# Optimization experiments

Measured on AMD Instinct MI355X. Metric: run time of the kernel, lower is better.

## Reference

```python
import jax, jax.numpy as jnp
import numpy as np

IN_F = 1024
OUT_F = 1024

def setup_inputs() -> dict:
    key = jax.random.key(0)
    ks = jax.random.split(key, 7)
    s = 1.0 / np.sqrt(IN_F)
    x = jax.random.normal(ks[0], (4, 2048, IN_F), dtype=jnp.float32)
    Wq = jax.random.uniform(ks[1], (OUT_F, IN_F), jnp.float32, -s, s)
    bq = jax.random.uniform(ks[2], (OUT_F,), jnp.float32, -s, s)
    Wk = jax.random.uniform(ks[3], (OUT_F, IN_F), jnp.float32, -s, s)
    bk = jax.random.uniform(ks[4], (OUT_F,), jnp.float32, -s, s)
    Wv = jax.random.uniform(ks[5], (OUT_F, IN_F), jnp.float32, -s, s)
    bv = jax.random.uniform(ks[6], (OUT_F,), jnp.float32, -s, s)
    return {"x": x, "Wq": Wq, "bq": bq, "Wk": Wk, "bk": bk, "Wv": Wv, "bv": bv}

def reference(x, Wq, bq, Wk, bk, Wv, bv):
    # Projector: ReLU(Linear(x))
    q = jax.nn.relu(jnp.einsum('bsd,od->bso', x, Wq) + bq)  # [B,S,O]
    k = jax.nn.relu(jnp.einsum('bsd,od->bso', x, Wk) + bk)
    v = jax.nn.relu(jnp.einsum('bsd,od->bso', x, Wv) + bv)
    logits = jnp.einsum('bio,bko->bik', q, k)  # unscaled QK^T, [B,S,S]
    scores = jax.nn.softmax(logits, axis=-1)
    out = jnp.einsum('bik,bko->bio', scores, v)
    return out
```

## Files before the change

kernel.cpp:

```cpp
#include <hip/hip_runtime.h>
#include <hip/hip_bf16.h>


#define SEQ 2048
#define DIM 1024
#define NB 4
#define MTOT (NB * SEQ)

typedef __attribute__((ext_vector_type(8))) short frag_ab;
typedef __attribute__((ext_vector_type(16))) float frag_c16;

__device__ __forceinline__ ushort f2bf(float f) {
    union { float f; unsigned u; } x; x.f = f;
    unsigned r = x.u + 0x7fffu + ((x.u >> 16) & 1u);
    return (ushort)(r >> 16);
}

typedef __attribute__((address_space(1))) const unsigned int guint;
typedef __attribute__((address_space(3))) unsigned int luint;

__device__ __forceinline__ void gld_lds16(const void* g, void* l) {
    __builtin_amdgcn_global_load_lds((guint*)g, (luint*)l, 16, 0, 0);
}

__device__ __forceinline__ void gemm_tiles(
    const ushort* __restrict__ A, size_t lda,
    const ushort* __restrict__ B, size_t ldb, int K,
    ushort* As, ushort* Bs, frag_c16 (&acc)[2][2])
{
    const int tid  = threadIdx.x;
    const int wave = tid >> 6;
    const int lane = tid & 63;
    const int l32  = lane & 31;
    const int half = lane >> 5;
    const int rin  = lane >> 3;
    const int cp   = lane & 7;
    const int cl   = cp ^ rin;
    const int wm = (wave & 1) * 64;
    const int wn = (wave >> 1) * 64;

    for (int k0 = 0; k0 < K; k0 += 64) {
        #pragma unroll
        for (int g = 0; g < 4; ++g) {
            int qc  = g * 4 + wave;
            int row = qc * 8 + rin;
            gld_lds16(A + (size_t)row * lda + k0 + cl * 8, As + qc * 512);
            gld_lds16(B + (size_t)row * ldb + k0 + cl * 8, Bs + qc * 512);
        }
        __syncthreads();
        frag_ab af[2][4], bf[2][4];
        #pragma unroll
        for (int mi = 0; mi < 2; ++mi) {
            int row = wm + mi * 32 + l32;
            int sw = row & 7;
            #pragma unroll
            for (int ks = 0; ks < 4; ++ks) {
                int c = (ks * 2 + half) ^ sw;
                af[mi][ks] = *(const frag_ab*)&As[row * 64 + c * 8];
            }
        }
        #pragma unroll
        for (int ni = 0; ni < 2; ++ni) {
            int row = wn + ni * 32 + l32;
            int sw = row & 7;
            #pragma unroll
            for (int ks = 0; ks < 4; ++ks) {
                int c = (ks * 2 + half) ^ sw;
                bf[ni][ks] = *(const frag_ab*)&Bs[row * 64 + c * 8];
            }
        }
        #pragma unroll
        for (int ks = 0; ks < 4; ++ks)
            #pragma unroll
            for (int mi = 0; mi < 2; ++mi)
                #pragma unroll
                for (int ni = 0; ni < 2; ++ni)
                    acc[mi][ni] = __builtin_amdgcn_mfma_f32_32x32x16_bf16(
                        af[mi][ks], bf[ni][ks], acc[mi][ni], 0, 0, 0);
        __syncthreads();
    }
}


#define NX4 (MTOT * DIM / 4)
#define NW4 (DIM * DIM / 4)
__global__ __launch_bounds__(256) void cvt_kernel(
    const float* __restrict__ x,
    const float* __restrict__ Wq, const float* __restrict__ Wk,
    const float* __restrict__ Wv,
    ushort* __restrict__ xb, ushort* __restrict__ Wb)
{
    size_t i = (size_t)blockIdx.x * 256 + threadIdx.x;
    const float* src; ushort* dst; size_t idx;
    if (i < NX4) { src = x; dst = xb; idx = i; }
    else {
        size_t j = i - NX4;
        int w = (int)(j >> 18);
        idx = j & (NW4 - 1);
        src = w == 0 ? Wq : (w == 1 ? Wk : Wv);
        dst = Wb + (size_t)w * DIM * DIM;
    }
    float4 f = ((const float4*)src)[idx];
    ushort4 u; u.x = f2bf(f.x); u.y = f2bf(f.y); u.z = f2bf(f.z); u.w = f2bf(f.w);
    ((ushort4*)dst)[idx] = u;
}

__global__ __launch_bounds__(256) void qkv_kernel(
    const ushort* __restrict__ xb, const ushort* __restrict__ Wb,
    const float* __restrict__ bq, const float* __restrict__ bk,
    const float* __restrict__ bv,
    ushort* __restrict__ q, ushort* __restrict__ kk, ushort* __restrict__ vt)
{
    const float* bias;
    if (blockIdx.z == 0)      bias = bq;
    else if (blockIdx.z == 1) bias = bk;
    else                      bias = bv;
    const ushort* W = Wb + (size_t)blockIdx.z * DIM * DIM;

    __shared__ ushort As[128 * 64];
    __shared__ ushort Bs[128 * 64];

    const int tid  = threadIdx.x;
    const int wave = tid >> 6;
    const int lane = tid & 63;
    const int l32  = lane & 31;
    const int half = lane >> 5;
    const int m0 = blockIdx.x * 128;
    const int n0 = blockIdx.y * 128;
    const int wm = (wave & 1) * 64;
    const int wn = (wave >> 1) * 64;

    frag_c16 acc[2][2] = {};
    gemm_tiles(xb + (size_t)m0 * DIM, DIM, W + (size_t)n0 * DIM, DIM, DIM,
               As, Bs, acc);

    if (blockIdx.z == 2) {
        const int bz = m0 >> 11;
        const int sb = (m0 & (SEQ - 1)) + wm;
        #pragma unroll
        for (int ni = 0; ni < 2; ++ni) {
            int col = n0 + wn + ni * 32 + l32;
            float bb = bias[col];
            ushort* vrow = vt + ((size_t)(bz * DIM + col)) * SEQ;
            #pragma unroll
            for (int mi = 0; mi < 2; ++mi)
                #pragma unroll
                for (int g = 0; g < 4; ++g) {
                    int s0 = sb + mi * 32 + 8 * g + 4 * half;
                    ushort4 u;
                    #pragma unroll
                    for (int j = 0; j < 4; ++j) {
                        float val = acc[mi][ni][4 * g + j] + bb;
                        val = val > 0.0f ? val : 0.0f;
                        ((ushort*)&u)[j] = f2bf(val);
                    }
                    *(ushort4*)&vrow[s0] = u;
                }
        }
    } else {
        ushort* out = blockIdx.z == 0 ? q : kk;
        #pragma unroll
        for (int ni = 0; ni < 2; ++ni) {
            int col = n0 + wn + ni * 32 + l32;
            float bb = bias[col];
            #pragma unroll
            for (int mi = 0; mi < 2; ++mi)
                #pragma unroll
                for (int r = 0; r < 16; ++r) {
                    int row = m0 + wm + mi * 32 + (r & 3) + 8 * (r >> 2) + 4 * half;
                    float val = acc[mi][ni][r] + bb;
                    val = val > 0.0f ? val : 0.0f;
                    out[(size_t)row * DIM + col] = f2bf(val);
                }
        }
    }
}

__global__ __launch_bounds__(256) void qk_kernel(
    const ushort* __restrict__ q, const ushort* __restrict__ kk,
    float* __restrict__ logits)
{
    __shared__ ushort As[128 * 64];
    __shared__ ushort Bs[128 * 64];

    const int tid  = threadIdx.x;
    const int wave = tid >> 6;
    const int lane = tid & 63;
    const int l32  = lane & 31;
    const int half = lane >> 5;
    const int bz = blockIdx.z;
    const int m0 = blockIdx.x * 128;
    const int n0 = blockIdx.y * 128;
    const int wm = (wave & 1) * 64;
    const int wn = (wave >> 1) * 64;
    const size_t base = (size_t)bz * SEQ;

    frag_c16 acc[2][2] = {};
    gemm_tiles(q + (base + m0) * DIM, DIM, kk + (base + n0) * DIM, DIM, DIM,
               As, Bs, acc);

    #pragma unroll
    for (int mi = 0; mi < 2; ++mi)
        #pragma unroll
        for (int r = 0; r < 16; ++r) {
            int row = m0 + wm + mi * 32 + (r & 3) + 8 * (r >> 2) + 4 * half;
            #pragma unroll
            for (int ni = 0; ni < 2; ++ni) {
                int col = n0 + wn + ni * 32 + l32;
                logits[(base + row) * SEQ + col] = acc[mi][ni][r];
            }
        }
}

__global__ __launch_bounds__(256) void softmax_kernel(float* __restrict__ logits)
{
    const int row  = blockIdx.x * 4 + (threadIdx.x >> 6);
    const int lane = threadIdx.x & 63;
    float* p = logits + (size_t)row * SEQ;

    float4 x[8];
    #pragma unroll
    for (int i = 0; i < 8; ++i) x[i] = ((const float4*)p)[lane + 64 * i];

    float m = -3.4e38f;
    #pragma unroll
    for (int i = 0; i < 8; ++i)
        m = fmaxf(m, fmaxf(fmaxf(x[i].x, x[i].y), fmaxf(x[i].z, x[i].w)));
    #pragma unroll
    for (int off = 32; off; off >>= 1) m = fmaxf(m, __shfl_xor(m, off, 64));

    float s = 0.0f;
    #pragma unroll
    for (int i = 0; i < 8; ++i) {
        x[i].x = __expf(x[i].x - m); x[i].y = __expf(x[i].y - m);
        x[i].z = __expf(x[i].z - m); x[i].w = __expf(x[i].w - m);
        s += (x[i].x + x[i].y) + (x[i].z + x[i].w);
    }
    #pragma unroll
    for (int off = 32; off; off >>= 1) s += __shfl_xor(s, off, 64);
    float inv = 1.0f / s;

    ushort* o = (ushort*)p;
    #pragma unroll
    for (int i = 0; i < 8; ++i) {
        ushort4 u;
        u.x = f2bf(x[i].x * inv); u.y = f2bf(x[i].y * inv);
        u.z = f2bf(x[i].z * inv); u.w = f2bf(x[i].w * inv);
        ((ushort4*)o)[lane + 64 * i] = u;
    }
}

__global__ __launch_bounds__(256) void pv_kernel(
    const ushort* __restrict__ probs, const ushort* __restrict__ vt,
    float* __restrict__ out)
{
    __shared__ ushort As[128 * 64];
    __shared__ ushort Bs[128 * 64];

    const int tid  = threadIdx.x;
    const int wave = tid >> 6;
    const int lane = tid & 63;
    const int l32  = lane & 31;
    const int half = lane >> 5;
    const int bz = blockIdx.z;
    const int m0 = blockIdx.x * 128;
    const int n0 = blockIdx.y * 128;
    const int wm = (wave & 1) * 64;
    const int wn = (wave >> 1) * 64;

    frag_c16 acc[2][2] = {};
    gemm_tiles(probs + ((size_t)(bz * SEQ + m0)) * 4096, 4096,
               vt + ((size_t)(bz * DIM + n0)) * SEQ, SEQ, SEQ,
               As, Bs, acc);

    #pragma unroll
    for (int mi = 0; mi < 2; ++mi)
        #pragma unroll
        for (int r = 0; r < 16; ++r) {
            int row = m0 + wm + mi * 32 + (r & 3) + 8 * (r >> 2) + 4 * half;
            #pragma unroll
            for (int ni = 0; ni < 2; ++ni) {
                int col = n0 + wn + ni * 32 + l32;
                out[((size_t)(bz * SEQ + row)) * DIM + col] = acc[mi][ni][r];
            }
        }
}

extern "C" void kernel_launch(void* const* d_in, const int* in_sizes, int n_in,
                              void* d_out, int out_size, void* d_ws, size_t ws_size,
                              hipStream_t stream)
{
    const float* x  = (const float*)d_in[0];
    const float* Wq = (const float*)d_in[1];
    const float* bq = (const float*)d_in[2];
    const float* Wk = (const float*)d_in[3];
    const float* bk = (const float*)d_in[4];
    const float* Wv = (const float*)d_in[5];
    const float* bv = (const float*)d_in[6];
    float* out = (float*)d_out;

    char* ws = (char*)d_ws;
    ushort* q      = (ushort*)(ws);
    ushort* kk     = (ushort*)(ws + ((size_t)16 << 20));
    ushort* vt     = (ushort*)(ws + ((size_t)48 << 20));
    float*  logits = (float*) (ws + ((size_t)64 << 20));
    ushort* xb     = (ushort*)(ws + ((size_t)64 << 20));
    ushort* Wb     = (ushort*)(ws + ((size_t)80 << 20));

    cvt_kernel<<<dim3((NX4 + 3 * NW4) / 256), 256, 0, stream>>>(
        x, Wq, Wk, Wv, xb, Wb);

    qkv_kernel<<<dim3(MTOT / 128, DIM / 128, 3), 256, 0, stream>>>(
        xb, Wb, bq, bk, bv, q, kk, vt);
    qk_kernel<<<dim3(SEQ / 128, SEQ / 128, NB), 256, 0, stream>>>(q, kk, logits);
    softmax_kernel<<<NB * SEQ / 4, 256, 0, stream>>>(logits);
    pv_kernel<<<dim3(SEQ / 128, DIM / 128, NB), 256, 0, stream>>>(
        (const ushort*)logits, vt, out);
}
```

Before: 265.3 us.

## Use 256x256 tiles with double-buffered async LDS pipeline in GEMM kernels

Replaces the 128x128 single-buffer GEMM core with a 256x256 tile computed by 8 waves, double-buffered LDS, and staged global-to-LDS loads issued ahead of the MFMA phases with explicit vmcnt waits and raw barriers. Wave priority is raised around MFMA bursts. The intent is to overlap memory loads with matrix math and to raise arithmetic intensity per tile. In exchange it uses 128KB of LDS per block, fewer blocks (grid shrinks 4x), and relies on hand-counted vmcnt ordering that could be fragile.

New measurement: 293.4 us. 10.6% more time.

```diff
diff --git a/kernel.cpp b/kernel.cpp
--- a/kernel.cpp
+++ b/kernel.cpp
@@ -23,62 +23,120 @@
     __builtin_amdgcn_global_load_lds((guint*)g, (luint*)l, 16, 0, 0);
 }
 
-__device__ __forceinline__ void gemm_tiles(
+__device__ __forceinline__ void bar() {
+    asm volatile("" ::: "memory");
+    __builtin_amdgcn_s_barrier();
+    asm volatile("" ::: "memory");
+}
+#define VMCNT(n) asm volatile("s_waitcnt vmcnt(" #n ")" ::: "memory")
+
+#define TS (256 * 64)
+
+__device__ __forceinline__ void stage64(const ushort* __restrict__ P,
+                                        size_t ld, int k0, ushort* dst,
+                                        int row0, int wave, int lane)
+{
+    int row = row0 + wave * 8 + (lane >> 3);
+    int cl  = (lane & 7) ^ (row & 7);
+    gld_lds16(P + (size_t)row * ld + k0 + cl * 8, dst + (row0 + wave * 8) * 64);
+}
+
+__device__ __forceinline__ void rdfrags(frag_ab (&f)[2][4], const ushort* S,
+                                        int r0, int l32, int half)
+{
+    #pragma unroll
+    for (int i = 0; i < 2; ++i) {
+        int row = r0 + i * 32 + l32;
+        int sw  = row & 7;
+        #pragma unroll
+        for (int ks = 0; ks < 4; ++ks)
+            f[i][ks] = *(const frag_ab*)&S[row * 64 + ((ks * 2 + half) ^ sw) * 8];
+    }
+}
+
+template<int MB>
+__device__ __forceinline__ void mfma16(frag_c16 (&acc)[4][2],
+                                       const frag_ab (&af)[2][4],
+                                       const frag_ab (&bf)[2][4])
+{
+    __builtin_amdgcn_s_setprio(1);
+    #pragma unroll
+    for (int ks = 0; ks < 4; ++ks)
+        #pragma unroll
+        for (int mi = 0; mi < 2; ++mi)
+            #pragma unroll
+            for (int ni = 0; ni < 2; ++ni)
+                acc[MB + mi][ni] = __builtin_amdgcn_mfma_f32_32x32x16_bf16(
+                    af[mi][ks], bf[ni][ks], acc[MB + mi][ni], 0, 0, 0);
+    __builtin_amdgcn_s_setprio(0);
+}
+
+__device__ __forceinline__ void gemm256(
     const ushort* __restrict__ A, size_t lda,
     const ushort* __restrict__ B, size_t ldb, int K,
-    ushort* As, ushort* Bs, frag_c16 (&acc)[2][2])
+    ushort (&Ab)[2][TS], ushort (&Bb)[2][TS], frag_c16 (&acc)[4][2])
 {
     const int tid  = threadIdx.x;
     const int wave = tid >> 6;
     const int lane = tid & 63;
     const int l32  = lane & 31;
     const int half = lane >> 5;
-    const int rin  = lane >> 3;
-    const int cp   = lane & 7;
-    const int cl   = cp ^ rin;
-    const int wm = (wave & 1) * 64;
-    const int wn = (wave >> 1) * 64;
-
-    for (int k0 = 0; k0 < K; k0 += 64) {
-        #pragma unroll
-        for (int g = 0; g < 4; ++g) {
-            int qc  = g * 4 + wave;
-            int row = qc * 8 + rin;
-            gld_lds16(A + (size_t)row * lda + k0 + cl * 8, As + qc * 512);
-            gld_lds16(B + (size_t)row * ldb + k0 + cl * 8, Bs + qc * 512);
-        }
-        __syncthreads();
+    const int wm   = (wave & 1) * 128;
+    const int wn   = (wave >> 1) * 64;
+    const int nkt  = K >> 6;
+
+    stage64(A, lda, 0, Ab[0], 0,   wave, lane);
+    stage64(A, lda, 0, Ab[0], 64,  wave, lane);
+    stage64(A, lda, 0, Ab[0], 128, wave, lane);
+    stage64(A, lda, 0, Ab[0], 192, wave, lane);
+    stage64(B, ldb, 0, Bb[0], 0,   wave, lane);
+    stage64(B, ldb, 0, Bb[0], 64,  wave, lane);
+    stage64(B, ldb, 0, Bb[0], 128, wave, lane);
+    stage64(B, ldb, 0, Bb[0], 192, wave, lane);
+    stage64(A, lda, 64, Ab[1], 0,   wave, lane);
+    stage64(A, lda, 64, Ab[1], 128, wave, lane);
+    stage64(B, ldb, 64, Bb[1], 0,   wave, lane);
+    stage64(B, ldb, 64, Bb[1], 64,  wave, lane);
+    stage64(B, ldb, 64, Bb[1], 128, wave, lane);
+    stage64(B, ldb, 64, Bb[1], 192, wave, lane);
+    VMCNT(6);
+    bar();
+
+    for (int t = 0; t < nkt; ++t) {
+        const int p = t & 1;
+        const ushort* Ap = Ab[p];
+        const ushort* Bp = Bb[p];
+
         frag_ab af[2][4], bf[2][4];
-        #pragma unroll
-        for (int mi = 0; mi < 2; ++mi) {
-            int row = wm + mi * 32 + l32;
-            int sw = row & 7;
-            #pragma unroll
-            for (int ks = 0; ks < 4; ++ks) {
-                int c = (ks * 2 + half) ^ sw;
-                af[mi][ks] = *(const frag_ab*)&As[row * 64 + c * 8];
-            }
-        }
-        #pragma unroll
-        for (int ni = 0; ni < 2; ++ni) {
-            int row = wn + ni * 32 + l32;
-            int sw = row & 7;
-            #pragma unroll
-            for (int ks = 0; ks < 4; ++ks) {
-                int c = (ks * 2 + half) ^ sw;
-                bf[ni][ks] = *(const frag_ab*)&Bs[row * 64 + c * 8];
-            }
-        }
-        #pragma unroll
-        for (int ks = 0; ks < 4; ++ks)
-            #pragma unroll
-            for (int mi = 0; mi < 2; ++mi)
-                #pragma unroll
-                for (int ni = 0; ni < 2; ++ni)
-                    acc[mi][ni] = __builtin_amdgcn_mfma_f32_32x32x16_bf16(
-                        af[mi][ks], bf[ni][ks], acc[mi][ni], 0, 0, 0);
-        __syncthreads();
-    }
+        rdfrags(af, Ap, wm, l32, half);
+        rdfrags(bf, Bp, wn, l32, half);
+        {
+            int k1 = (t + 1 < nkt ? t + 1 : nkt - 1) * 64;
+            stage64(A, lda, k1, Ab[p ^ 1], 64,  wave, lane);
+            stage64(A, lda, k1, Ab[p ^ 1], 192, wave, lane);
+        }
+        bar();
+        mfma16<0>(acc, af, bf);
+        VMCNT(8);
+        bar();
+
+        frag_ab ag[2][4];
+        rdfrags(ag, Ap, wm + 64, l32, half);
+        {
+            int k2 = (t + 2 < nkt ? t + 2 : nkt - 1) * 64;
+            stage64(A, lda, k2, Ab[p], 0,   wave, lane);
+            stage64(A, lda, k2, Ab[p], 128, wave, lane);
+            stage64(B, ldb, k2, Bb[p], 0,   wave, lane);
+            stage64(B, ldb, k2, Bb[p], 64,  wave, lane);
+            stage64(B, ldb, k2, Bb[p], 128, wave, lane);
+            stage64(B, ldb, k2, Bb[p], 192, wave, lane);
+        }
+        bar();
+        mfma16<2>(acc, ag, bf);
+        VMCNT(8);
+        bar();
+    }
+    VMCNT(0);
 }
 
 
@@ -105,34 +163,35 @@
     ((ushort4*)dst)[idx] = u;
 }
 
-__global__ __launch_bounds__(256) void qkv_kernel(
+__global__ __launch_bounds__(512, 2) void qkv_kernel(
     const ushort* __restrict__ xb, const ushort* __restrict__ Wb,
     const float* __restrict__ bq, const float* __restrict__ bk,
     const float* __restrict__ bv,
     ushort* __restrict__ q, ushort* __restrict__ kk, ushort* __restrict__ vt)
 {
+    __shared__ ushort Ab[2][TS];
+    __shared__ ushort Bb[2][TS];
+
     const float* bias;
     if (blockIdx.z == 0)      bias = bq;
     else if (blockIdx.z == 1) bias = bk;
     else                      bias = bv;
     const ushort* W = Wb + (size_t)blockIdx.z * DIM * DIM;
 
-    __shared__ ushort As[128 * 64];
-    __shared__ ushort Bs[128 * 64];
+    const int m0 = blockIdx.x * 256;
+    const int n0 = blockIdx.y * 256;
+
+    frag_c16 acc[4][2] = {};
+    gemm256(xb + (size_t)m0 * DIM, DIM, W + (size_t)n0 * DIM, DIM, DIM,
+            Ab, Bb, acc);
 
     const int tid  = threadIdx.x;
     const int wave = tid >> 6;
     const int lane = tid & 63;
     const int l32  = lane & 31;
     const int half = lane >> 5;
-    const int m0 = blockIdx.x * 128;
-    const int n0 = blockIdx.y * 128;
-    const int wm = (wave & 1) * 64;
-    const int wn = (wave >> 1) * 64;
-
-    frag_c16 acc[2][2] = {};
-    gemm_tiles(xb + (size_t)m0 * DIM, DIM, W + (size_t)n0 * DIM, DIM, DIM,
-               As, Bs, acc);
+    const int wm   = (wave & 1) * 128;
+    const int wn   = (wave >> 1) * 64;
 
     if (blockIdx.z == 2) {
         const int bz = m0 >> 11;
@@ -143,7 +202,7 @@
             float bb = bias[col];
             ushort* vrow = vt + ((size_t)(bz * DIM + col)) * SEQ;
             #pragma unroll
-            for (int mi = 0; mi < 2; ++mi)
+            for (int mi = 0; mi < 4; ++mi)
                 #pragma unroll
                 for (int g = 0; g < 4; ++g) {
                     int s0 = sb + mi * 32 + 8 * g + 4 * half;
@@ -164,7 +223,7 @@
             int col = n0 + wn + ni * 32 + l32;
             float bb = bias[col];
             #pragma unroll
-            for (int mi = 0; mi < 2; ++mi)
+            for (int mi = 0; mi < 4; ++mi)
                 #pragma unroll
                 for (int r = 0; r < 16; ++r) {
                     int row = m0 + wm + mi * 32 + (r & 3) + 8 * (r >> 2) + 4 * half;
@@ -176,31 +235,32 @@
     }
 }
 
-__global__ __launch_bounds__(256) void qk_kernel(
+__global__ __launch_bounds__(512, 2) void qk_kernel(
     const ushort* __restrict__ q, const ushort* __restrict__ kk,
     float* __restrict__ logits)
 {
-    __shared__ ushort As[128 * 64];
-    __shared__ ushort Bs[128 * 64];
+    __shared__ ushort Ab[2][TS];
+    __shared__ ushort Bb[2][TS];
+
+    const int bz = blockIdx.z;
+    const int m0 = blockIdx.x * 256;
+    const int n0 = blockIdx.y * 256;
+    const size_t base = (size_t)bz * SEQ;
+
+    frag_c16 acc[4][2] = {};
+    gemm256(q + (base + m0) * DIM, DIM, kk + (base + n0) * DIM, DIM, DIM,
+            Ab, Bb, acc);
 
     const int tid  = threadIdx.x;
     const int wave = tid >> 6;
     const int lane = tid & 63;
     const int l32  = lane & 31;
     const int half = lane >> 5;
-    const int bz = blockIdx.z;
-    const int m0 = blockIdx.x * 128;
-    const int n0 = blockIdx.y * 128;
-    const int wm = (wave & 1) * 64;
-    const int wn = (wave >> 1) * 64;
-    const size_t base = (size_t)bz * SEQ;
-
-    frag_c16 acc[2][2] = {};
-    gemm_tiles(q + (base + m0) * DIM, DIM, kk + (base + n0) * DIM, DIM, DIM,
-               As, Bs, acc);
-
-    #pragma unroll
-    for (int mi = 0; mi < 2; ++mi)
+    const int wm   = (wave & 1) * 128;
+    const int wn   = (wave >> 1) * 64;
+
+    #pragma unroll
+    for (int mi = 0; mi < 4; ++mi)
         #pragma unroll
         for (int r = 0; r < 16; ++r) {
             int row = m0 + wm + mi * 32 + (r & 3) + 8 * (r >> 2) + 4 * half;
@@ -250,31 +310,32 @@
     }
 }
 
-__global__ __launch_bounds__(256) void pv_kernel(
+__global__ __launch_bounds__(512, 2) void pv_kernel(
     const ushort* __restrict__ probs, const ushort* __restrict__ vt,
     float* __restrict__ out)
 {
-    __shared__ ushort As[128 * 64];
-    __shared__ ushort Bs[128 * 64];
+    __shared__ ushort Ab[2][TS];
+    __shared__ ushort Bb[2][TS];
+
+    const int bz = blockIdx.z;
+    const int m0 = blockIdx.x * 256;
+    const int n0 = blockIdx.y * 256;
+
+    frag_c16 acc[4][2] = {};
+    gemm256(probs + ((size_t)(bz * SEQ + m0)) * 4096, 4096,
+            vt + ((size_t)(bz * DIM + n0)) * SEQ, SEQ, SEQ,
+            Ab, Bb, acc);
 
     const int tid  = threadIdx.x;
     const int wave = tid >> 6;
     const int lane = tid & 63;
     const int l32  = lane & 31;
     const int half = lane >> 5;
-    const int bz = blockIdx.z;
-    const int m0 = blockIdx.x * 128;
-    const int n0 = blockIdx.y * 128;
-    const int wm = (wave & 1) * 64;
-    const int wn = (wave >> 1) * 64;
-
-    frag_c16 acc[2][2] = {};
-    gemm_tiles(probs + ((size_t)(bz * SEQ + m0)) * 4096, 4096,
-               vt + ((size_t)(bz * DIM + n0)) * SEQ, SEQ, SEQ,
-               As, Bs, acc);
-
-    #pragma unroll
-    for (int mi = 0; mi < 2; ++mi)
+    const int wm   = (wave & 1) * 128;
+    const int wn   = (wave >> 1) * 64;
+
+    #pragma unroll
+    for (int mi = 0; mi < 4; ++mi)
         #pragma unroll
         for (int r = 0; r < 16; ++r) {
             int row = m0 + wm + mi * 32 + (r & 3) + 8 * (r >> 2) + 4 * half;
@@ -310,10 +371,10 @@
     cvt_kernel<<<dim3((NX4 + 3 * NW4) / 256), 256, 0, stream>>>(
         x, Wq, Wk, Wv, xb, Wb);
 
-    qkv_kernel<<<dim3(MTOT / 128, DIM / 128, 3), 256, 0, stream>>>(
+    qkv_kernel<<<dim3(MTOT / 256, DIM / 256, 3), 512, 0, stream>>>(
         xb, Wb, bq, bk, bv, q, kk, vt);
-    qk_kernel<<<dim3(SEQ / 128, SEQ / 128, NB), 256, 0, stream>>>(q, kk, logits);
+    qk_kernel<<<dim3(SEQ / 256, SEQ / 256, NB), 512, 0, stream>>>(q, kk, logits);
     softmax_kernel<<<NB * SEQ / 4, 256, 0, stream>>>(logits);
-    pv_kernel<<<dim3(SEQ / 128, DIM / 128, NB), 256, 0, stream>>>(
+    pv_kernel<<<dim3(SEQ / 256, DIM / 256, NB), 512, 0, stream>>>(
         (const ushort*)logits, vt, out);
 }
```
